# Optimization experiments

Hardware: AMD Instinct MI355X
Metric: run time of the kernel (lower is better)

Reference implementation:

```python
import jax, jax.numpy as jnp
import numpy as np

DIM = 1024
HEADS = 16
DIM_HEAD = 64
INNER = HEADS * DIM_HEAD  # 1024
RANK = 16
ALPHA = 8.0
LORA_SCALE = ALPHA / RANK  # 0.5
NUM_PATCHES = 256
NUM_FRAMES = 8
T = NUM_PATCHES * NUM_FRAMES  # 2048
B = 2
MEM = 16
EPS = 1e-5


def _block_causal_mask(num_patches, num_frames):
    # generate_mask_matrix: causal across frames, full within a frame
    tril = np.tril(np.ones((num_frames, num_frames), dtype=np.int32))
    m = np.kron(tril, np.ones((num_patches, num_patches), dtype=np.int32))
    return jnp.asarray(m[None, None])  # [1,1,T,T]


def setup_inputs() -> dict:
    key = jax.random.key(0)
    ks = jax.random.split(key, 16)
    s_in = 1.0 / np.sqrt(DIM)
    s_r = 1.0 / np.sqrt(RANK)
    return {
        "x": jax.random.normal(ks[0], (B, T, DIM), jnp.float32),
        "memory_tokens": jax.random.normal(ks[1], (B, MEM, DIM), jnp.float32),
        "ln_g": jnp.ones((DIM,), jnp.float32),
        "ln_b": jnp.zeros((DIM,), jnp.float32),
        "w_qkv": jax.random.normal(ks[2], (DIM, 3 * INNER), jnp.float32) * s_in,
        "qA": jax.random.normal(ks[3], (DIM, RANK), jnp.float32) * s_in,
        "qB": jax.random.normal(ks[4], (RANK, INNER), jnp.float32) * s_r * 0.02,
        "kA": jax.random.normal(ks[5], (DIM, RANK), jnp.float32) * s_in,
        "kB": jax.random.normal(ks[6], (RANK, INNER), jnp.float32) * s_r * 0.02,
        "vA": jax.random.normal(ks[7], (DIM, RANK), jnp.float32) * s_in,
        "vB": jax.random.normal(ks[8], (RANK, INNER), jnp.float32) * s_r * 0.02,
        "w_out": jax.random.normal(ks[9], (INNER, DIM), jnp.float32) / np.sqrt(INNER),
        "b_out": jnp.zeros((DIM,), jnp.float32),
        "outA": jax.random.normal(ks[10], (INNER, RANK), jnp.float32) / np.sqrt(INNER),
        "outB": jax.random.normal(ks[11], (RANK, DIM), jnp.float32) * s_r * 0.02,
        "bias_mask": _block_causal_mask(NUM_PATCHES, NUM_FRAMES),
    }


def _lora(x, A, Bm):
    return LORA_SCALE * ((x @ A) @ Bm)


def reference(x, memory_tokens, ln_g, ln_b, w_qkv, qA, qB, kA, kB, vA, vB,
              w_out, b_out, outA, outB, bias_mask):
    # LayerNorm
    mu = jnp.mean(x, axis=-1, keepdims=True)
    var = jnp.var(x, axis=-1, keepdims=True)
    xn = (x - mu) * jax.lax.rsqrt(var + EPS) * ln_g + ln_b

    qkv = xn @ w_qkv  # [B,T,3*INNER]
    q, k, v = jnp.split(qkv, 3, axis=-1)
    # LoRA deltas (memory_tokens enables the LoRA path)
    q = q + _lora(xn, qA, qB)
    k = k + _lora(xn, kA, kB)
    v = v + _lora(xn, vA, vB)

    def to_heads(t):
        b, n, _ = t.shape
        return t.reshape(b, n, HEADS, DIM_HEAD).transpose(0, 2, 1, 3)  # b h n d

    q, k, v = to_heads(q), to_heads(k), to_heads(v)
    scale = DIM_HEAD ** -0.5
    dots = jnp.einsum('bhid,bhjd->bhij', q, k) * scale  # [B,H,T,T]
    dots = jnp.where(bias_mask[:, :, :q.shape[2], :q.shape[2]] == 0, -jnp.inf, dots)
    attn = jax.nn.softmax(dots, axis=-1)  # dropout p=0.0
    out = jnp.einsum('bhij,bhjd->bhid', attn, v)
    out = out.transpose(0, 2, 1, 3).reshape(x.shape[0], x.shape[1], INNER)
    out = out @ w_out + b_out
    out = out + _lora(out, outA, outB)  # lora_on_out
    return out
```

## Files before the change

kernel.cpp:

```cpp
#include <hip/hip_runtime.h>


#define DIMSZ 1024
#define TSEQ  2048
#define MTOK  4096

typedef __attribute__((ext_vector_type(8))) short bf16x8;
typedef __attribute__((ext_vector_type(4))) short bf16x4;
typedef __attribute__((ext_vector_type(4))) float f32x4;

__device__ __forceinline__ unsigned short f2bf(float f) {
  unsigned int u = __float_as_uint(f);
  u += 0x7fffu + ((u >> 16) & 1u);
  return (unsigned short)(u >> 16);
}
__device__ __forceinline__ float bf2f(unsigned short s) {
  return __uint_as_float(((unsigned int)s) << 16);
}
__device__ __forceinline__ unsigned int cvtpk_bf16(float a, float b) {
  unsigned int d;
  asm("v_cvt_pk_bf16_f32 %0, %1, %2" : "=v"(d) : "v"(a), "v"(b));
  return d;
}
__device__ __forceinline__ void gload16(const void* g, void* l) {
  __builtin_amdgcn_global_load_lds((const __attribute__((address_space(1))) void*)g,
                                   (__attribute__((address_space(3))) void*)l, 16, 0, 0);
}

__global__ __launch_bounds__(256) void prep_kernel(const float* __restrict__ x,
    const float* __restrict__ g, const float* __restrict__ bln,
    const float* __restrict__ w_out, const float* __restrict__ outA,
    const float* __restrict__ b_out, const float* __restrict__ outB,
    unsigned short* __restrict__ xn, float* __restrict__ WA,
    float* __restrict__ beff) {
  __shared__ float red[8];
  __shared__ float sh[4][16];
  __shared__ float tt[16];
  int bid = blockIdx.x;
  int tid = threadIdx.x, wid = tid >> 6, lane = tid & 63;
  if (bid < MTOK) {
    int row = bid;
    const float4* xr = (const float4*)(x + (size_t)row * DIMSZ);
    float4 v = xr[tid];
    float s  = v.x + v.y + v.z + v.w;
    float s2 = v.x*v.x + v.y*v.y + v.z*v.z + v.w*v.w;
    #pragma unroll
    for (int off = 32; off > 0; off >>= 1) {
      s  += __shfl_xor(s, off, 64);
      s2 += __shfl_xor(s2, off, 64);
    }
    if (lane == 0) { red[wid] = s; red[wid + 4] = s2; }
    __syncthreads();
    s  = red[0] + red[1] + red[2] + red[3];
    s2 = red[4] + red[5] + red[6] + red[7];
    float mu  = s * (1.0f / DIMSZ);
    float var = s2 * (1.0f / DIMSZ) - mu * mu;
    float rstd = rsqrtf(var + 1e-5f);
    float4 gg = ((const float4*)g)[tid];
    float4 bb = ((const float4*)bln)[tid];
    ushort4 o;
    o.x = f2bf((v.x - mu) * rstd * gg.x + bb.x);
    o.y = f2bf((v.y - mu) * rstd * gg.y + bb.y);
    o.z = f2bf((v.z - mu) * rstd * gg.z + bb.z);
    o.w = f2bf((v.w - mu) * rstd * gg.w + bb.w);
    ((ushort4*)(xn + (size_t)row * DIMSZ))[tid] = o;
  } else if (bid < MTOK + 256) {
    int k = (bid - MTOK) * 4 + wid;
    float a[16];
    #pragma unroll
    for (int r = 0; r < 16; ++r) a[r] = 0.f;
    for (int c = lane; c < DIMSZ; c += 64) {
      float w = w_out[(size_t)k * DIMSZ + c];
      const float* ap = outA + (size_t)c * 16;
      #pragma unroll
      for (int r = 0; r < 16; ++r) a[r] += w * ap[r];
    }
    #pragma unroll
    for (int r = 0; r < 16; ++r) {
      #pragma unroll
      for (int off = 32; off > 0; off >>= 1) a[r] += __shfl_xor(a[r], off, 64);
    }
    if (lane < 16) WA[k * 16 + lane] = a[lane];
  } else {
    float a[16];
    #pragma unroll
    for (int r = 0; r < 16; ++r) a[r] = 0.f;
    for (int c = tid; c < DIMSZ; c += 256) {
      float bo = b_out[c];
      const float* ap = outA + (size_t)c * 16;
      #pragma unroll
      for (int r = 0; r < 16; ++r) a[r] += bo * ap[r];
    }
    #pragma unroll
    for (int r = 0; r < 16; ++r) {
      #pragma unroll
      for (int off = 32; off > 0; off >>= 1) a[r] += __shfl_xor(a[r], off, 64);
    }
    if (lane == 0) {
      #pragma unroll
      for (int r = 0; r < 16; ++r) sh[wid][r] = a[r];
    }
    __syncthreads();
    if (tid < 16) tt[tid] = sh[0][tid] + sh[1][tid] + sh[2][tid] + sh[3][tid];
    __syncthreads();
    for (int n = tid; n < DIMSZ; n += 256) {
      float l = 0.f;
      #pragma unroll
      for (int r = 0; r < 16; ++r) l += tt[r] * outB[(size_t)r * DIMSZ + n];
      beff[n] = b_out[n] + 0.5f * l;
    }
  }
}

__global__ __launch_bounds__(256) void foldT4_kernel(
    const float* __restrict__ w_qkv, const float* __restrict__ w_out,
    const float* __restrict__ qA, const float* __restrict__ qB,
    const float* __restrict__ kA, const float* __restrict__ kB,
    const float* __restrict__ vA, const float* __restrict__ vB,
    const float* __restrict__ WA, const float* __restrict__ outB,
    unsigned short* __restrict__ WqkvT, unsigned short* __restrict__ WoutT) {
  __shared__ float Bs[16][64];
  __shared__ unsigned short Ts[64][72];
  int z = blockIdx.z;
  const float *W, *A, *Bf;
  unsigned short* Wt;
  int ldw, col_off;
  if (z == 0)      { W = w_qkv; ldw = 3072; col_off = 0;    A = qA; Bf = qB;   Wt = WqkvT; }
  else if (z == 1) { W = w_qkv; ldw = 3072; col_off = 1024; A = kA; Bf = kB;   Wt = WqkvT + 1048576; }
  else if (z == 2) { W = w_qkv; ldw = 3072; col_off = 2048; A = vA; Bf = vB;   Wt = WqkvT + 2097152; }
  else             { W = w_out; ldw = 1024; col_off = 0;    A = WA; Bf = outB; Wt = WoutT; }
  int n0 = blockIdx.x * 64, k0 = blockIdx.y * 64;
  int tx = threadIdx.x, ty = threadIdx.y;
  for (int r = ty; r < 16; r += 4) Bs[r][tx] = Bf[(size_t)r * DIMSZ + n0 + tx];
  __syncthreads();
  for (int k = ty; k < 64; k += 4) {
    int kk = k0 + k;
    float w = W[(size_t)kk * ldw + col_off + n0 + tx];
    const float* Ar = A + (size_t)kk * 16;
    float lora = 0.f;
    #pragma unroll
    for (int r = 0; r < 16; ++r) lora += Ar[r] * Bs[r][tx];
    Ts[tx][k] = f2bf(w + 0.5f * lora);
  }
  __syncthreads();
  for (int n = ty; n < 64; n += 4)
    Wt[(size_t)(n0 + n) * DIMSZ + k0 + tx] = Ts[n][tx];
}

template<int MODE>
__global__ __launch_bounds__(256) void gemm_kernel(
    const unsigned short* __restrict__ Abf, const unsigned short* __restrict__ Bt,
    int K,
    unsigned short* __restrict__ Qo, unsigned short* __restrict__ Ko,
    unsigned short* __restrict__ Vto,
    const float* __restrict__ bias, float* __restrict__ Cout) {
  __shared__ __align__(16) char As[128 * 64 * 2];
  __shared__ __align__(16) char Bs[128 * 64 * 2];
  int nwg = gridDim.x * gridDim.y;
  int lin = blockIdx.y * gridDim.x + blockIdx.x;
  int cpx = nwg >> 3;
  int swz = (lin & 7) * cpx + (lin >> 3);
  int bx = swz % gridDim.x;
  int by = swz / gridDim.x;
  int n0 = bx * 128;
  int m0 = by * 128;
  int tid = threadIdx.x;
  int wid = tid >> 6, lane = tid & 63;
  int wr = wid >> 1, wc = wid & 1;
  int hi = lane >> 4;
  f32x4 acc[4][4];
  #pragma unroll
  for (int i = 0; i < 4; ++i)
    #pragma unroll
    for (int j = 0; j < 4; ++j) acc[i][j] = (f32x4){0.f, 0.f, 0.f, 0.f};

  const char* gA = (const char*)Abf;
  const char* gB = (const char*)Bt;
  int Kb2 = K * 2;
  int nkt = K >> 6;
  for (int kt = 0; kt < nkt; ++kt) {
    #pragma unroll
    for (int j = 0; j < 4; ++j) {
      int it = wid * 4 + j;
      int p = it * 1024 + lane * 16;
      int row = p >> 7, colb = p & 127;
      int L = colb ^ ((row & 7) << 4);
      gload16(gA + (size_t)(m0 + row) * Kb2 + kt * 128 + L, As + it * 1024);
      gload16(gB + (size_t)(n0 + row) * Kb2 + kt * 128 + L, Bs + it * 1024);
    }
    __syncthreads();
    #pragma unroll
    for (int ks = 0; ks < 2; ++ks) {
      int kb = ks * 64 + hi * 16;
      bf16x8 af[4], bfr[4];
      #pragma unroll
      for (int m = 0; m < 4; ++m) {
        int row = wr * 64 + m * 16 + (lane & 15);
        af[m] = *(const bf16x8*)(As + row * 128 + (kb ^ ((row & 7) << 4)));
      }
      #pragma unroll
      for (int n = 0; n < 4; ++n) {
        int row = wc * 64 + n * 16 + (lane & 15);
        bfr[n] = *(const bf16x8*)(Bs + row * 128 + (kb ^ ((row & 7) << 4)));
      }
      __builtin_amdgcn_s_setprio(1);
      #pragma unroll
      for (int n = 0; n < 4; ++n)
        #pragma unroll
        for (int m = 0; m < 4; ++m)
          acc[n][m] = __builtin_amdgcn_mfma_f32_16x16x32_bf16(bfr[n], af[m], acc[n][m], 0, 0, 0);
      __builtin_amdgcn_s_setprio(0);
    }
    __syncthreads();
  }

  if (MODE == 0) {
    int sec  = n0 >> 10;
    int nloc = (n0 & 1023) + wc * 64;
    int h = nloc >> 6;
    int mbase = m0 + wr * 64;
    #pragma unroll
    for (int m = 0; m < 4; ++m) {
      int gm = mbase + m * 16 + (lane & 15);
      int bb = gm >> 11, t = gm & 2047;
      #pragma unroll
      for (int n = 0; n < 4; ++n) {
        int dloc = n * 16 + hi * 4;
        if (sec == 2) {
          #pragma unroll
          for (int r = 0; r < 4; ++r)
            Vto[((size_t)((bb * 16 + h) * 64 + dloc + r)) * TSEQ + t] = f2bf(acc[n][m][r]);
        } else {
          bf16x4 o;
          #pragma unroll
          for (int r = 0; r < 4; ++r) o[r] = (short)f2bf(acc[n][m][r]);
          size_t idx = ((size_t)(bb * 16 + h) * TSEQ + t) * 64 + dloc;
          *(bf16x4*)((sec == 0 ? Qo : Ko) + idx) = o;
        }
      }
    }
  } else {
    int mbase = m0 + wr * 64;
    int nbase = n0 + wc * 64;
    #pragma unroll
    for (int m = 0; m < 4; ++m) {
      int t = mbase + m * 16 + (lane & 15);
      #pragma unroll
      for (int n = 0; n < 4; ++n) {
        int c = nbase + n * 16 + hi * 4;
        float4 bs = *(const float4*)(bias + c);
        float4 o;
        o.x = acc[n][m][0] + bs.x;
        o.y = acc[n][m][1] + bs.y;
        o.z = acc[n][m][2] + bs.z;
        o.w = acc[n][m][3] + bs.w;
        *(float4*)(Cout + (size_t)t * DIMSZ + c) = o;
      }
    }
  }
}

__global__ __launch_bounds__(256, 4) void attn_kernel(
    const unsigned short* __restrict__ Qg, const unsigned short* __restrict__ Kg,
    const unsigned short* __restrict__ Vt, unsigned short* __restrict__ Orow) {
  __shared__ __align__(16) char KsB[2][64 * 128];
  __shared__ __align__(16) char VsB[2][64 * 128];
  __shared__ __align__(16) char Ps[4][16 * 128];
  int bh = blockIdx.x;
  int y  = blockIdx.y;
  int qt = (y < 16) ? (31 - y) : (y - 16);
  int b = bh >> 4, h = bh & 15;
  int tid = threadIdx.x, wid = tid >> 6, lane = tid & 63;
  int hi = lane >> 4, lo = lane & 15;
  const char* Qb = (const char*)(Qg + (size_t)bh * TSEQ * 64);
  const char* Kb = (const char*)(Kg + (size_t)bh * TSEQ * 64);
  const char* Vb = (const char*)(Vt + (size_t)bh * 64 * TSEQ);
  int q0 = qt * 64;

  int srow = tid >> 3;
  int scol = ((tid & 7) << 4) ^ ((srow & 7) << 4);

  const float qscale = 0.18033688f;
  bf16x8 qf[2];
  {
    int row = q0 + wid * 16 + lo;
    #pragma unroll
    for (int ks = 0; ks < 2; ++ks) {
      bf16x8 raw = *(const bf16x8*)(Qb + (size_t)row * 128 + ks * 64 + hi * 16);
      bf16x8 sc;
      #pragma unroll
      for (int i = 0; i < 8; ++i)
        sc[i] = (short)f2bf(bf2f((unsigned short)raw[i]) * qscale);
      qf[ks] = sc;
    }
  }

  f32x4 Oacc[4];
  #pragma unroll
  for (int df = 0; df < 4; ++df) Oacc[df] = (f32x4){0.f, 0.f, 0.f, 0.f};
  float mrun = -INFINITY, lrun = 0.f;

  char* Pw = Ps[wid];
  char* pbase = Pw + lo * 128;
  int pswz = (lo & 7) << 4;

  int nkt = ((qt >> 2) + 1) << 2;

  {
    const char* ksrc = Kb + (size_t)srow * 128 + scol;
    gload16(ksrc,               KsB[0] + tid * 16);
    gload16(ksrc + 32 * 128,    KsB[0] + tid * 16 + 4096);
    const char* vsrc = Vb + (size_t)srow * (TSEQ * 2) + scol;
    gload16(vsrc,               VsB[0] + tid * 16);
    gload16(vsrc + 32 * (TSEQ * 2), VsB[0] + tid * 16 + 4096);
  }

  for (int kt = 0; kt < nkt; ++kt) {
    __syncthreads();
    if (kt + 1 < nkt) {
      int k0n = (kt + 1) << 6;
      char* kd = KsB[(kt + 1) & 1];
      const char* ksrc = Kb + (size_t)(k0n + srow) * 128 + scol;
      gload16(ksrc,            kd + tid * 16);
      gload16(ksrc + 32 * 128, kd + tid * 16 + 4096);
    }
    if (kt) {
      char* vd = VsB[kt & 1];
      const char* vsrc = Vb + (size_t)srow * (TSEQ * 2) + (kt << 7) + scol;
      gload16(vsrc,                   vd + tid * 16);
      gload16(vsrc + 32 * (TSEQ * 2), vd + tid * 16 + 4096);
    }
    const char* Kbuf = KsB[kt & 1];

    f32x4 s[4];
    #pragma unroll
    for (int nf = 0; nf < 4; ++nf) s[nf] = (f32x4){0.f, 0.f, 0.f, 0.f};
    #pragma unroll
    for (int ks = 0; ks < 2; ++ks) {
      int kb = ks * 64 + hi * 16;
      bf16x8 kf[4];
      #pragma unroll
      for (int nf = 0; nf < 4; ++nf) {
        int row = nf * 16 + lo;
        kf[nf] = *(const bf16x8*)(Kbuf + row * 128 + (kb ^ ((row & 7) << 4)));
      }
      __builtin_amdgcn_s_setprio(1);
      #pragma unroll
      for (int nf = 0; nf < 4; ++nf)
        s[nf] = __builtin_amdgcn_mfma_f32_16x16x32_bf16(kf[nf], qf[ks], s[nf], 0, 0, 0);
      __builtin_amdgcn_s_setprio(0);
    }

    if (kt) {
      const char* Vbuf = VsB[(kt - 1) & 1];
      #pragma unroll
      for (int ks2 = 0; ks2 < 2; ++ks2) {
        int kb = ks2 * 64 + hi * 16;
        bf16x8 pf = *(const bf16x8*)(Pw + lo * 128 + (kb ^ pswz));
        bf16x8 vf[4];
        #pragma unroll
        for (int df = 0; df < 4; ++df) {
          int row = df * 16 + lo;
          vf[df] = *(const bf16x8*)(Vbuf + row * 128 + (kb ^ ((row & 7) << 4)));
        }
        __builtin_amdgcn_s_setprio(1);
        #pragma unroll
        for (int df = 0; df < 4; ++df)
          Oacc[df] = __builtin_amdgcn_mfma_f32_16x16x32_bf16(vf[df], pf, Oacc[df], 0, 0, 0);
        __builtin_amdgcn_s_setprio(0);
      }
    }

    float a0 = fmaxf(fmaxf(s[0][0], s[0][1]), fmaxf(s[0][2], s[0][3]));
    float a1 = fmaxf(fmaxf(s[1][0], s[1][1]), fmaxf(s[1][2], s[1][3]));
    float a2 = fmaxf(fmaxf(s[2][0], s[2][1]), fmaxf(s[2][2], s[2][3]));
    float a3 = fmaxf(fmaxf(s[3][0], s[3][1]), fmaxf(s[3][2], s[3][3]));
    float mx = fmaxf(fmaxf(a0, a1), fmaxf(a2, a3));
    mx = fmaxf(mx, __shfl_xor(mx, 16, 64));
    mx = fmaxf(mx, __shfl_xor(mx, 32, 64));

    if (!__all(mx <= mrun + 8.0f)) {
      float mn = fmaxf(mrun, mx);
      float al = exp2f(mrun - mn);
      mrun = mn;
      lrun *= al;
      #pragma unroll
      for (int df = 0; df < 4; ++df)
        #pragma unroll
        for (int r = 0; r < 4; ++r) Oacc[df][r] *= al;
    }

    float rs0 = 0.f, rs1 = 0.f, rs2 = 0.f, rs3 = 0.f;
    #pragma unroll
    for (int nf = 0; nf < 4; ++nf) {
      float p0 = exp2f(s[nf][0] - mrun);
      float p1 = exp2f(s[nf][1] - mrun);
      float p2 = exp2f(s[nf][2] - mrun);
      float p3 = exp2f(s[nf][3] - mrun);
      s[nf][0] = p0; s[nf][1] = p1; s[nf][2] = p2; s[nf][3] = p3;
      rs0 += p0; rs1 += p1; rs2 += p2; rs3 += p3;
    }
    lrun += (rs0 + rs1) + (rs2 + rs3);

    #pragma unroll
    for (int nf = 0; nf < 4; ++nf) {
      unsigned int w0 = cvtpk_bf16(s[nf][0], s[nf][1]);
      unsigned int w1 = cvtpk_bf16(s[nf][2], s[nf][3]);
      uint2 pr; pr.x = w0; pr.y = w1;
      *(uint2*)(pbase + ((nf * 32 + hi * 8) ^ pswz)) = pr;
    }
  }

  __syncthreads();
  {
    const char* Vbuf = VsB[(nkt - 1) & 1];
    #pragma unroll
    for (int ks2 = 0; ks2 < 2; ++ks2) {
      int kb = ks2 * 64 + hi * 16;
      bf16x8 pf = *(const bf16x8*)(Pw + lo * 128 + (kb ^ pswz));
      bf16x8 vf[4];
      #pragma unroll
      for (int df = 0; df < 4; ++df) {
        int row = df * 16 + lo;
        vf[df] = *(const bf16x8*)(Vbuf + row * 128 + (kb ^ ((row & 7) << 4)));
      }
      __builtin_amdgcn_s_setprio(1);
      #pragma unroll
      for (int df = 0; df < 4; ++df)
        Oacc[df] = __builtin_amdgcn_mfma_f32_16x16x32_bf16(vf[df], pf, Oacc[df], 0, 0, 0);
      __builtin_amdgcn_s_setprio(0);
    }
  }

  lrun += __shfl_xor(lrun, 16, 64);
  lrun += __shfl_xor(lrun, 32, 64);
  float inv = 1.0f / lrun;
  int t = q0 + wid * 16 + lo;
  size_t rowbase = ((size_t)(b * TSEQ + t)) * DIMSZ + h * 64;
  #pragma unroll
  for (int df = 0; df < 4; ++df) {
    bf16x4 o;
    #pragma unroll
    for (int r = 0; r < 4; ++r) o[r] = (short)f2bf(Oacc[df][r] * inv);
    *(bf16x4*)(Orow + rowbase + df * 16 + hi * 4) = o;
  }
}

extern "C" void kernel_launch(void* const* d_in, const int* in_sizes, int n_in,
                              void* d_out, int out_size, void* d_ws, size_t ws_size,
                              hipStream_t stream) {
  (void)in_sizes; (void)n_in; (void)out_size; (void)ws_size;
  const float* x     = (const float*)d_in[0];
  const float* ln_g  = (const float*)d_in[2];
  const float* ln_b  = (const float*)d_in[3];
  const float* w_qkv = (const float*)d_in[4];
  const float* qA    = (const float*)d_in[5];
  const float* qB    = (const float*)d_in[6];
  const float* kA    = (const float*)d_in[7];
  const float* kB    = (const float*)d_in[8];
  const float* vA    = (const float*)d_in[9];
  const float* vB    = (const float*)d_in[10];
  const float* w_out = (const float*)d_in[11];
  const float* b_out = (const float*)d_in[12];
  const float* outA  = (const float*)d_in[13];
  const float* outB  = (const float*)d_in[14];

  char* ws = (char*)d_ws;
  unsigned short* xn    = (unsigned short*)(ws);
  unsigned short* WqkvT = (unsigned short*)(ws + 8388608);
  unsigned short* WoutT = (unsigned short*)(ws + 14680064);
  float*          WA    = (float*)(ws + 16777216);
  float*          beff  = (float*)(ws + 16842752);
  unsigned short* Qb    = (unsigned short*)(ws + 16846848);
  unsigned short* Kb    = (unsigned short*)(ws + 25235456);
  unsigned short* Vtb   = (unsigned short*)(ws + 33624064);
  unsigned short* Orow  = xn;
  float* outp = (float*)d_out;

  prep_kernel<<<MTOK + 257, 256, 0, stream>>>(x, ln_g, ln_b, w_out, outA, b_out,
                                              outB, xn, WA, beff);
  dim3 fb(64, 4);
  foldT4_kernel<<<dim3(16, 16, 4), fb, 0, stream>>>(w_qkv, w_out, qA, qB, kA, kB,
                                                    vA, vB, WA, outB, WqkvT, WoutT);

  gemm_kernel<0><<<dim3(24, 32), 256, 0, stream>>>(xn, WqkvT, DIMSZ, Qb, Kb, Vtb, nullptr, nullptr);
  attn_kernel<<<dim3(32, 32), 256, 0, stream>>>(Qb, Kb, Vtb, Orow);
  gemm_kernel<1><<<dim3(8, 32), 256, 0, stream>>>(Orow, WoutT, DIMSZ, nullptr, nullptr, nullptr, beff, outp);
}
```

Baseline: 138.7 us.

## Split long causal attention tiles across key ranges and merge partials

Query tiles 20-31 each have their key range split into two jobs, taken from a static job table. Each job writes fp16 partial outputs plus log-sum-exp stats, and a new merge kernel combines each pair into bf16 rows. This balances work across the 44 job slots so the longest blocks no longer set the kernel tail. The cost is an extra kernel launch, partial-output traffic that reuses the WqkvT workspace, and fp16 precision for the partial outputs.

```diff
diff --git a/kernel.cpp b/kernel.cpp
--- a/kernel.cpp
+++ b/kernel.cpp
@@ -21,6 +21,16 @@
   unsigned int d;
   asm("v_cvt_pk_bf16_f32 %0, %1, %2" : "=v"(d) : "v"(a), "v"(b));
   return d;
+}
+__device__ __forceinline__ unsigned int cvtpk_f16(float a, float b) {
+  unsigned int d;
+  asm("v_cvt_pkrtz_f16_f32 %0, %1, %2" : "=v"(d) : "v"(a), "v"(b));
+  return d;
+}
+__device__ __forceinline__ float h2f(unsigned int hbits) {
+  float f;
+  asm("v_cvt_f32_f16 %0, %1" : "=v"(f) : "v"(hbits));
+  return f;
 }
 __device__ __forceinline__ void gload16(const void* g, void* l) {
   __builtin_amdgcn_global_load_lds((const __attribute__((address_space(1))) void*)g,
@@ -260,15 +270,31 @@
   }
 }
 
+#define J(qt, kb, ke) ((qt) | ((kb) << 8) | ((ke) << 16))
+__device__ const int JOBS[44] = {
+  J(16,0,20), J(17,0,20), J(18,0,20), J(19,0,20),
+  J(12,0,16), J(13,0,16), J(14,0,16), J(15,0,16),
+  J(28,0,16), J(28,16,32), J(29,0,16), J(29,16,32),
+  J(30,0,16), J(30,16,32), J(31,0,16), J(31,16,32),
+  J(24,0,14), J(24,14,28), J(25,0,14), J(25,14,28),
+  J(26,0,14), J(26,14,28), J(27,0,14), J(27,14,28),
+  J(8,0,12), J(9,0,12), J(10,0,12), J(11,0,12),
+  J(20,0,12), J(20,12,24), J(21,0,12), J(21,12,24),
+  J(22,0,12), J(22,12,24), J(23,0,12), J(23,12,24),
+  J(4,0,8), J(5,0,8), J(6,0,8), J(7,0,8),
+  J(0,0,4), J(1,0,4), J(2,0,4), J(3,0,4)
+};
+
 __global__ __launch_bounds__(256, 4) void attn_kernel(
     const unsigned short* __restrict__ Qg, const unsigned short* __restrict__ Kg,
-    const unsigned short* __restrict__ Vt, unsigned short* __restrict__ Orow) {
+    const unsigned short* __restrict__ Vt, unsigned short* __restrict__ Orow,
+    char* __restrict__ Opart, float* __restrict__ Lstat) {
   __shared__ __align__(16) char KsB[2][64 * 128];
   __shared__ __align__(16) char VsB[2][64 * 128];
   __shared__ __align__(16) char Ps[4][16 * 128];
   int bh = blockIdx.x;
-  int y  = blockIdx.y;
-  int qt = (y < 16) ? (31 - y) : (y - 16);
+  int job = JOBS[blockIdx.y];
+  int qt = job & 0xff, ktb = (job >> 8) & 0xff, kte = (job >> 16) & 0xff;
   int b = bh >> 4, h = bh & 15;
   int tid = threadIdx.x, wid = tid >> 6, lane = tid & 63;
   int hi = lane >> 4, lo = lane & 15;
@@ -304,27 +330,26 @@
   char* pbase = Pw + lo * 128;
   int pswz = (lo & 7) << 4;
 
-  int nkt = ((qt >> 2) + 1) << 2;
-
   {
-    const char* ksrc = Kb + (size_t)srow * 128 + scol;
-    gload16(ksrc,               KsB[0] + tid * 16);
-    gload16(ksrc + 32 * 128,    KsB[0] + tid * 16 + 4096);
-    const char* vsrc = Vb + (size_t)srow * (TSEQ * 2) + scol;
-    gload16(vsrc,               VsB[0] + tid * 16);
-    gload16(vsrc + 32 * (TSEQ * 2), VsB[0] + tid * 16 + 4096);
-  }
-
-  for (int kt = 0; kt < nkt; ++kt) {
+    char* kd = KsB[ktb & 1];
+    char* vd = VsB[ktb & 1];
+    const char* ksrc = Kb + (size_t)((ktb << 6) + srow) * 128 + scol;
+    gload16(ksrc,            kd + tid * 16);
+    gload16(ksrc + 32 * 128, kd + tid * 16 + 4096);
+    const char* vsrc = Vb + (size_t)srow * (TSEQ * 2) + (ktb << 7) + scol;
+    gload16(vsrc,                   vd + tid * 16);
+    gload16(vsrc + 32 * (TSEQ * 2), vd + tid * 16 + 4096);
+  }
+
+  for (int kt = ktb; kt < kte; ++kt) {
     __syncthreads();
-    if (kt + 1 < nkt) {
-      int k0n = (kt + 1) << 6;
+    if (kt + 1 < kte) {
       char* kd = KsB[(kt + 1) & 1];
-      const char* ksrc = Kb + (size_t)(k0n + srow) * 128 + scol;
+      const char* ksrc = Kb + (size_t)(((kt + 1) << 6) + srow) * 128 + scol;
       gload16(ksrc,            kd + tid * 16);
       gload16(ksrc + 32 * 128, kd + tid * 16 + 4096);
     }
-    if (kt) {
+    if (kt != ktb) {
       char* vd = VsB[kt & 1];
       const char* vsrc = Vb + (size_t)srow * (TSEQ * 2) + (kt << 7) + scol;
       gload16(vsrc,                   vd + tid * 16);
@@ -351,7 +376,7 @@
       __builtin_amdgcn_s_setprio(0);
     }
 
-    if (kt) {
+    if (kt != ktb) {
       const char* Vbuf = VsB[(kt - 1) & 1];
       #pragma unroll
       for (int ks2 = 0; ks2 < 2; ++ks2) {
@@ -413,7 +438,7 @@
 
   __syncthreads();
   {
-    const char* Vbuf = VsB[(nkt - 1) & 1];
+    const char* Vbuf = VsB[(kte - 1) & 1];
     #pragma unroll
     for (int ks2 = 0; ks2 < 2; ++ks2) {
       int kb = ks2 * 64 + hi * 16;
@@ -435,15 +460,67 @@
   lrun += __shfl_xor(lrun, 16, 64);
   lrun += __shfl_xor(lrun, 32, 64);
   float inv = 1.0f / lrun;
-  int t = q0 + wid * 16 + lo;
-  size_t rowbase = ((size_t)(b * TSEQ + t)) * DIMSZ + h * 64;
+  int q = wid * 16 + lo;
+  if (qt >= 20) {
+    int p = bh * 24 + ((qt - 20) << 1) + (ktb ? 1 : 0);
+    char* Op = Opart + (size_t)p * 8192 + q * 128;
+    #pragma unroll
+    for (int df = 0; df < 4; ++df) {
+      uint2 w;
+      w.x = cvtpk_f16(Oacc[df][0] * inv, Oacc[df][1] * inv);
+      w.y = cvtpk_f16(Oacc[df][2] * inv, Oacc[df][3] * inv);
+      *(uint2*)(Op + df * 32 + hi * 8) = w;
+    }
+    if (hi == 0) Lstat[p * 64 + q] = mrun + __log2f(lrun);
+  } else {
+    int t = q0 + q;
+    size_t rowbase = ((size_t)(b * TSEQ + t)) * DIMSZ + h * 64;
+    #pragma unroll
+    for (int df = 0; df < 4; ++df) {
+      bf16x4 o;
+      #pragma unroll
+      for (int r = 0; r < 4; ++r) o[r] = (short)f2bf(Oacc[df][r] * inv);
+      *(bf16x4*)(Orow + rowbase + df * 16 + hi * 4) = o;
+    }
+  }
+}
+
+__global__ __launch_bounds__(256) void merge_kernel(
+    const char* __restrict__ Opart, const float* __restrict__ Lstat,
+    unsigned short* __restrict__ Orow) {
+  int j = blockIdx.x, bh = blockIdx.y;
+  int qt = 20 + j;
+  int b = bh >> 4, h = bh & 15;
+  int pA = bh * 24 + j * 2, pB = pA + 1;
+  int t = threadIdx.x;
+  int q = t >> 2, d0 = (t & 3) << 4;
+  float LA = Lstat[pA * 64 + q], LB = Lstat[pB * 64 + q];
+  float Lm = fmaxf(LA, LB);
+  float wA = exp2f(LA - Lm), wB = exp2f(LB - Lm);
+  float inv = 1.0f / (wA + wB);
+  wA *= inv; wB *= inv;
+  const char* pa = Opart + (size_t)pA * 8192 + q * 128 + d0 * 2;
+  const char* pb = Opart + (size_t)pB * 8192 + q * 128 + d0 * 2;
+  uint4 a0 = *(const uint4*)pa;
+  uint4 a1 = *(const uint4*)(pa + 16);
+  uint4 b0 = *(const uint4*)pb;
+  uint4 b1 = *(const uint4*)(pb + 16);
+  unsigned int oc[8];
+  const unsigned int* au = (const unsigned int*)&a0;
+  unsigned int av[8] = {a0.x, a0.y, a0.z, a0.w, a1.x, a1.y, a1.z, a1.w};
+  unsigned int bv[8] = {b0.x, b0.y, b0.z, b0.w, b1.x, b1.y, b1.z, b1.w};
+  (void)au;
   #pragma unroll
-  for (int df = 0; df < 4; ++df) {
-    bf16x4 o;
-    #pragma unroll
-    for (int r = 0; r < 4; ++r) o[r] = (short)f2bf(Oacc[df][r] * inv);
-    *(bf16x4*)(Orow + rowbase + df * 16 + hi * 4) = o;
-  }
+  for (int i = 0; i < 8; ++i) {
+    float f0 = wA * h2f(av[i] & 0xffffu) + wB * h2f(bv[i] & 0xffffu);
+    float f1 = wA * h2f(av[i] >> 16)     + wB * h2f(bv[i] >> 16);
+    oc[i] = cvtpk_bf16(f0, f1);
+  }
+  size_t off = ((size_t)(b * TSEQ + qt * 64 + q)) * DIMSZ + h * 64 + d0;
+  uint4 o0; o0.x = oc[0]; o0.y = oc[1]; o0.z = oc[2]; o0.w = oc[3];
+  uint4 o1; o1.x = oc[4]; o1.y = oc[5]; o1.z = oc[6]; o1.w = oc[7];
+  *(uint4*)(Orow + off) = o0;
+  *(uint4*)(Orow + off + 8) = o1;
 }
 
 extern "C" void kernel_launch(void* const* d_in, const int* in_sizes, int n_in,
@@ -474,6 +551,8 @@
   unsigned short* Qb    = (unsigned short*)(ws + 16846848);
   unsigned short* Kb    = (unsigned short*)(ws + 25235456);
   unsigned short* Vtb   = (unsigned short*)(ws + 33624064);
+  float*          Lstat = (float*)(ws + 42012672);
+  char*           Opart = (char*)WqkvT;
   unsigned short* Orow  = xn;
   float* outp = (float*)d_out;
 
@@ -484,6 +563,7 @@
                                                     vA, vB, WA, outB, WqkvT, WoutT);
 
   gemm_kernel<0><<<dim3(24, 32), 256, 0, stream>>>(xn, WqkvT, DIMSZ, Qb, Kb, Vtb, nullptr, nullptr);
-  attn_kernel<<<dim3(32, 32), 256, 0, stream>>>(Qb, Kb, Vtb, Orow);
+  attn_kernel<<<dim3(32, 44), 256, 0, stream>>>(Qb, Kb, Vtb, Orow, Opart, Lstat);
+  merge_kernel<<<dim3(12, 32), 256, 0, stream>>>(Opart, Lstat, Orow);
   gemm_kernel<1><<<dim3(8, 32), 256, 0, stream>>>(Orow, WoutT, DIMSZ, nullptr, nullptr, nullptr, beff, outp);
 }
```

New measurement: 141.6 us. 1.02x slower.

## Fold LoRA weight-merge blocks into prep and QKV GEMM launches, drop separate fold kernel

Applied to the files above, without the earlier changes.

Removes the standalone foldT4 kernel. The QKV weight folding now runs as extra blocks in the prep (LayerNorm) launch, and the output-weight folding runs as extra blocks appended to the QKV GEMM launch, since it only depends on WA from prep. This removes one kernel launch and its serialization gap, and overlaps the fold work with LN and GEMM work. The cost is heavier, heterogeneous blocks inside those launches, with possible tail imbalance and more register or LDS pressure in the GEMM.

```diff
diff --git a/kernel.cpp b/kernel.cpp
--- a/kernel.cpp
+++ b/kernel.cpp
@@ -31,8 +31,12 @@
     const float* __restrict__ g, const float* __restrict__ bln,
     const float* __restrict__ w_out, const float* __restrict__ outA,
     const float* __restrict__ b_out, const float* __restrict__ outB,
+    const float* __restrict__ w_qkv,
+    const float* __restrict__ qA, const float* __restrict__ qB,
+    const float* __restrict__ kA, const float* __restrict__ kB,
+    const float* __restrict__ vA, const float* __restrict__ vB,
     unsigned short* __restrict__ xn, float* __restrict__ WA,
-    float* __restrict__ beff) {
+    float* __restrict__ beff, unsigned short* __restrict__ WqkvT) {
   __shared__ float red[8];
   __shared__ float sh[4][16];
   __shared__ float tt[16];
@@ -81,7 +85,7 @@
       for (int off = 32; off > 0; off >>= 1) a[r] += __shfl_xor(a[r], off, 64);
     }
     if (lane < 16) WA[k * 16 + lane] = a[lane];
-  } else {
+  } else if (bid == MTOK + 256) {
     float a[16];
     #pragma unroll
     for (int r = 0; r < 16; ++r) a[r] = 0.f;
@@ -109,42 +113,34 @@
       for (int r = 0; r < 16; ++r) l += tt[r] * outB[(size_t)r * DIMSZ + n];
       beff[n] = b_out[n] + 0.5f * l;
     }
-  }
-}
-
-__global__ __launch_bounds__(256) void foldT4_kernel(
-    const float* __restrict__ w_qkv, const float* __restrict__ w_out,
-    const float* __restrict__ qA, const float* __restrict__ qB,
-    const float* __restrict__ kA, const float* __restrict__ kB,
-    const float* __restrict__ vA, const float* __restrict__ vB,
-    const float* __restrict__ WA, const float* __restrict__ outB,
-    unsigned short* __restrict__ WqkvT, unsigned short* __restrict__ WoutT) {
-  __shared__ float Bs[16][64];
-  __shared__ unsigned short Ts[64][72];
-  int z = blockIdx.z;
-  const float *W, *A, *Bf;
-  unsigned short* Wt;
-  int ldw, col_off;
-  if (z == 0)      { W = w_qkv; ldw = 3072; col_off = 0;    A = qA; Bf = qB;   Wt = WqkvT; }
-  else if (z == 1) { W = w_qkv; ldw = 3072; col_off = 1024; A = kA; Bf = kB;   Wt = WqkvT + 1048576; }
-  else if (z == 2) { W = w_qkv; ldw = 3072; col_off = 2048; A = vA; Bf = vB;   Wt = WqkvT + 2097152; }
-  else             { W = w_out; ldw = 1024; col_off = 0;    A = WA; Bf = outB; Wt = WoutT; }
-  int n0 = blockIdx.x * 64, k0 = blockIdx.y * 64;
-  int tx = threadIdx.x, ty = threadIdx.y;
-  for (int r = ty; r < 16; r += 4) Bs[r][tx] = Bf[(size_t)r * DIMSZ + n0 + tx];
-  __syncthreads();
-  for (int k = ty; k < 64; k += 4) {
-    int kk = k0 + k;
-    float w = W[(size_t)kk * ldw + col_off + n0 + tx];
-    const float* Ar = A + (size_t)kk * 16;
-    float lora = 0.f;
-    #pragma unroll
-    for (int r = 0; r < 16; ++r) lora += Ar[r] * Bs[r][tx];
-    Ts[tx][k] = f2bf(w + 0.5f * lora);
-  }
-  __syncthreads();
-  for (int n = ty; n < 64; n += 4)
-    Wt[(size_t)(n0 + n) * DIMSZ + k0 + tx] = Ts[n][tx];
+  } else {
+    __shared__ float Bsf[16][64];
+    __shared__ unsigned short Ts[64][72];
+    int fid = bid - (MTOK + 257);
+    int z = fid >> 8, rem = fid & 255;
+    int n0 = (rem & 15) * 64, k0 = (rem >> 4) * 64;
+    const float *A, *Bf;
+    unsigned short* Wt;
+    if (z == 0)      { A = qA; Bf = qB; Wt = WqkvT; }
+    else if (z == 1) { A = kA; Bf = kB; Wt = WqkvT + 1048576; }
+    else             { A = vA; Bf = vB; Wt = WqkvT + 2097152; }
+    int coff = z << 10;
+    int tx = tid & 63, ty = tid >> 6;
+    for (int r = ty; r < 16; r += 4) Bsf[r][tx] = Bf[(size_t)r * DIMSZ + n0 + tx];
+    __syncthreads();
+    for (int k = ty; k < 64; k += 4) {
+      int kk = k0 + k;
+      float w = w_qkv[(size_t)kk * 3072 + coff + n0 + tx];
+      const float* Ar = A + (size_t)kk * 16;
+      float lora = 0.f;
+      #pragma unroll
+      for (int r = 0; r < 16; ++r) lora += Ar[r] * Bsf[r][tx];
+      Ts[tx][k] = f2bf(w + 0.5f * lora);
+    }
+    __syncthreads();
+    for (int n = ty; n < 64; n += 4)
+      Wt[(size_t)(n0 + n) * DIMSZ + k0 + tx] = Ts[n][tx];
+  }
 }
 
 template<int MODE>
@@ -153,18 +149,43 @@
     int K,
     unsigned short* __restrict__ Qo, unsigned short* __restrict__ Ko,
     unsigned short* __restrict__ Vto,
-    const float* __restrict__ bias, float* __restrict__ Cout) {
+    const float* __restrict__ bias, float* __restrict__ Cout,
+    const float* __restrict__ w_out, const float* __restrict__ WAf,
+    const float* __restrict__ outB, unsigned short* __restrict__ WoutT) {
   __shared__ __align__(16) char As[128 * 64 * 2];
   __shared__ __align__(16) char Bs[128 * 64 * 2];
-  int nwg = gridDim.x * gridDim.y;
-  int lin = blockIdx.y * gridDim.x + blockIdx.x;
-  int cpx = nwg >> 3;
+  int lin = blockIdx.x;
+  int tid = threadIdx.x;
+  if (MODE == 0 && lin >= 768) {
+    float (*Bsf)[64] = (float(*)[64])As;
+    unsigned short (*Ts)[72] = (unsigned short(*)[72])(As + 4096);
+    int rem = lin - 768;
+    int n0 = (rem & 15) * 64, k0 = (rem >> 4) * 64;
+    int tx = tid & 63, ty = tid >> 6;
+    for (int r = ty; r < 16; r += 4) Bsf[r][tx] = outB[(size_t)r * DIMSZ + n0 + tx];
+    __syncthreads();
+    for (int k = ty; k < 64; k += 4) {
+      int kk = k0 + k;
+      float w = w_out[(size_t)kk * DIMSZ + n0 + tx];
+      const float* Ar = WAf + (size_t)kk * 16;
+      float lora = 0.f;
+      #pragma unroll
+      for (int r = 0; r < 16; ++r) lora += Ar[r] * Bsf[r][tx];
+      Ts[tx][k] = f2bf(w + 0.5f * lora);
+    }
+    __syncthreads();
+    for (int n = ty; n < 64; n += 4)
+      WoutT[(size_t)(n0 + n) * DIMSZ + k0 + tx] = Ts[n][tx];
+    return;
+  }
+  const int ngemm = (MODE == 0) ? 768 : 256;
+  const int gx    = (MODE == 0) ? 24 : 8;
+  int cpx = ngemm >> 3;
   int swz = (lin & 7) * cpx + (lin >> 3);
-  int bx = swz % gridDim.x;
-  int by = swz / gridDim.x;
+  int bx = swz % gx;
+  int by = swz / gx;
   int n0 = bx * 128;
   int m0 = by * 128;
-  int tid = threadIdx.x;
   int wid = tid >> 6, lane = tid & 63;
   int wr = wid >> 1, wc = wid & 1;
   int hi = lane >> 4;
@@ -477,13 +498,11 @@
   unsigned short* Orow  = xn;
   float* outp = (float*)d_out;
 
-  prep_kernel<<<MTOK + 257, 256, 0, stream>>>(x, ln_g, ln_b, w_out, outA, b_out,
-                                              outB, xn, WA, beff);
-  dim3 fb(64, 4);
-  foldT4_kernel<<<dim3(16, 16, 4), fb, 0, stream>>>(w_qkv, w_out, qA, qB, kA, kB,
-                                                    vA, vB, WA, outB, WqkvT, WoutT);
-
-  gemm_kernel<0><<<dim3(24, 32), 256, 0, stream>>>(xn, WqkvT, DIMSZ, Qb, Kb, Vtb, nullptr, nullptr);
+  prep_kernel<<<MTOK + 257 + 768, 256, 0, stream>>>(x, ln_g, ln_b, w_out, outA,
+      b_out, outB, w_qkv, qA, qB, kA, kB, vA, vB, xn, WA, beff, WqkvT);
+  gemm_kernel<0><<<1024, 256, 0, stream>>>(xn, WqkvT, DIMSZ, Qb, Kb, Vtb,
+      nullptr, nullptr, w_out, WA, outB, WoutT);
   attn_kernel<<<dim3(32, 32), 256, 0, stream>>>(Qb, Kb, Vtb, Orow);
-  gemm_kernel<1><<<dim3(8, 32), 256, 0, stream>>>(Orow, WoutT, DIMSZ, nullptr, nullptr, nullptr, beff, outp);
-}
+  gemm_kernel<1><<<256, 256, 0, stream>>>(Orow, WoutT, DIMSZ, nullptr, nullptr,
+      nullptr, beff, outp, nullptr, nullptr, nullptr, nullptr);
+}
```

After: 130.9 us. 5.6% less time.
